# Kernel tuning notes

Measured on AMD Instinct MI355X. Metric: run time of the kernel, lower is better.

The kernel has to match this reference:

```python
import jax, jax.numpy as jnp
import numpy as np

N_CONCEPT = 15000  # graph has N_CONCEPT + 1 nodes
NNZ = 240016
EPS = 1e-12  # F.normalize eps


def setup_inputs() -> dict:
    key = jax.random.key(0)
    ks = jax.random.split(key, 10)
    B, S, E, O, D = 2048, 32, 1024, 1024, 1024
    s = 1.0 / np.sqrt(E)
    return {
        "data": jax.random.normal(ks[0], (B, S, E), jnp.float32),
        "seq_len": jax.random.randint(ks[1], (B,), 1, S + 1, jnp.int32),
        "conv_w": jax.random.normal(ks[2], (O, E), jnp.float32) * s,
        "conv_b": jax.random.normal(ks[3], (O,), jnp.float32) * s,
        "lin_w": jax.random.normal(ks[4], (D, O), jnp.float32) * s,
        "lin_b": jax.random.normal(ks[5], (D,), jnp.float32) * s,
        "gcn_bias": jnp.zeros((D,), jnp.float32),
        "H0": jax.random.normal(ks[6], (N_CONCEPT + 1, D), jnp.float32) * s,
        "indices": jax.random.randint(ks[7], (2, NNZ), 0, N_CONCEPT + 1, jnp.int32),
        "values": jax.random.uniform(ks[8], (NNZ,), jnp.float32),
    }


def reference(data, seq_len, conv_w, conv_b, lin_w, lin_b, gcn_bias, H0, indices, values):
    # --- CNN phrase encoder ---
    # conv1d kernel_size=1 == per-token linear: (B,S,E)x(O,E) -> (B,S,O)
    x = jax.nn.relu(jnp.einsum("bse,oe->bso", data, conv_w) + conv_b)
    x = jnp.max(x, axis=1)                              # max over sequence -> (B,O)
    x = jax.nn.relu(x @ lin_w.T + lin_b)                # (B,D)
    norm = jnp.linalg.norm(x, axis=1, keepdims=True)
    phrase = x / jnp.maximum(norm, EPS)                 # L2 normalize

    # --- sparse Laplacian GCN: L @ H0 + bias ---
    rows, cols = indices[0], indices[1]
    msgs = values[:, None] * H0[cols]                   # (nnz, D)
    graph = jax.ops.segment_sum(msgs, rows, num_segments=N_CONCEPT + 1) + gcn_bias

    # --- bilinear score: (B,D) @ (D, N+1) ---
    logits = phrase @ graph.T
    return logits
```

## Files before the change

kernel.cpp:

```cpp
#include <hip/hip_runtime.h>
#include <stdint.h>

typedef __attribute__((ext_vector_type(8))) __bf16 bf16x8;
typedef __attribute__((ext_vector_type(4))) float floatx4;

#define GLOBAL_AS __attribute__((address_space(1)))
#define LDS_AS __attribute__((address_space(3)))

#define CAP 96
#define N1 15001
#define NPAD 15104

__device__ __forceinline__ unsigned short f2bf(float x) {
  unsigned int u = __builtin_bit_cast(unsigned int, x);
  u += 0x7FFFu + ((u >> 16) & 1u);
  return (unsigned short)(u >> 16);
}
__device__ __forceinline__ unsigned int pk2(float lo, float hi) {
  return (unsigned)f2bf(lo) | ((unsigned)f2bf(hi) << 16);
}

__device__ __forceinline__ void stage_tile(const unsigned short* g, int ld, int row0, int k0,
                                           bf16x8* lds, int tid) {
  const int lane = tid & 63;
  const int w = tid >> 6;
#pragma unroll
  for (int j = 0; j < 2; ++j) {
    const int c = j * 256 + w * 64;
    const int kg = c >> 7;
    const int mbase = c & 127;
    const unsigned short* src = g + ((size_t)(row0 + mbase + lane) * ld + k0 + kg * 8);
    __builtin_amdgcn_global_load_lds((const GLOBAL_AS void*)src, (LDS_AS void*)(lds + c),
                                     16, 0, 0);
  }
}

template <int MODE>
__launch_bounds__(256, 2)
__global__ void gemm_bt(const void* __restrict__ Aptr,
                        const unsigned short* __restrict__ Bm,
                        const float* __restrict__ bias,
                        float* __restrict__ outF,
                        unsigned short* __restrict__ outU,
                        int nValid) {
  __shared__ bf16x8 As[512];
  __shared__ bf16x8 Bs[512];
  const int tid = threadIdx.x;
  const int lane = tid & 63;
  const int w = tid >> 6;
  const int wm = w >> 1, wn = w & 1;
  const int quad = lane >> 4, col = lane & 15;
  const int m0 = blockIdx.y * 128, n0 = blockIdx.x * 128;
  const int K = 1024;

  floatx4 acc[4][4];
#pragma unroll
  for (int a = 0; a < 4; ++a)
#pragma unroll
    for (int b = 0; b < 4; ++b) acc[a][b] = 0;

  for (int k0 = 0; k0 < K; k0 += 32) {
    __syncthreads();
    if (MODE == 0) {
      const int row = tid >> 1, kh = tid & 1;
      const float* src = (const float*)Aptr + (size_t)(m0 + row) * K + k0 + kh * 16;
      float4 v0 = ((const float4*)src)[0];
      float4 v1 = ((const float4*)src)[1];
      float4 v2 = ((const float4*)src)[2];
      float4 v3 = ((const float4*)src)[3];
      stage_tile(Bm, K, n0, k0, Bs, tid);
      uint4 c0, c1;
      c0.x = pk2(v0.x, v0.y); c0.y = pk2(v0.z, v0.w);
      c0.z = pk2(v1.x, v1.y); c0.w = pk2(v1.z, v1.w);
      c1.x = pk2(v2.x, v2.y); c1.y = pk2(v2.z, v2.w);
      c1.z = pk2(v3.x, v3.y); c1.w = pk2(v3.z, v3.w);
      ((uint4*)As)[(kh * 2) * 128 + row] = c0;
      ((uint4*)As)[(kh * 2 + 1) * 128 + row] = c1;
    } else {
      stage_tile((const unsigned short*)Aptr, K, m0, k0, As, tid);
      stage_tile(Bm, K, n0, k0, Bs, tid);
    }
    __syncthreads();
    bf16x8 af[4], bfr[4];
#pragma unroll
    for (int t = 0; t < 4; ++t) af[t] = As[quad * 128 + wm * 64 + t * 16 + col];
#pragma unroll
    for (int t = 0; t < 4; ++t) bfr[t] = Bs[quad * 128 + wn * 64 + t * 16 + col];
#pragma unroll
    for (int mt = 0; mt < 4; ++mt)
#pragma unroll
      for (int nt = 0; nt < 4; ++nt)
        acc[mt][nt] = __builtin_amdgcn_mfma_f32_16x16x32_bf16(af[mt], bfr[nt], acc[mt][nt], 0, 0, 0);
  }

  if (MODE == 0 || MODE == 3) {
    float bv[4];
#pragma unroll
    for (int nt = 0; nt < 4; ++nt) bv[nt] = bias[n0 + wn * 64 + nt * 16 + col];
#pragma unroll
    for (int g = 0; g < 2; ++g) {
#pragma unroll
      for (int nt = 0; nt < 4; ++nt) {
        float v = -3.4e38f;
#pragma unroll
        for (int mh = 0; mh < 2; ++mh) {
          const int mt = 2 * g + mh;
#pragma unroll
          for (int r = 0; r < 4; ++r) v = fmaxf(v, acc[mt][nt][r]);
        }
        v += bv[nt];
        v = fmaxf(v, __shfl_xor(v, 16, 64));
        v = fmaxf(v, __shfl_xor(v, 32, 64));
        v = fmaxf(v, 0.0f);
        if (quad == 0) {
          const int b = (m0 >> 5) + wm * 2 + g;
          outU[b * 1024 + n0 + wn * 64 + nt * 16 + col] = f2bf(v);
        }
      }
    }
  } else if (MODE == 1) {
    float bv[4];
#pragma unroll
    for (int nt = 0; nt < 4; ++nt) bv[nt] = bias[n0 + wn * 64 + nt * 16 + col];
#pragma unroll
    for (int mt = 0; mt < 4; ++mt)
#pragma unroll
      for (int r = 0; r < 4; ++r) {
        const int row = m0 + wm * 64 + mt * 16 + quad * 4 + r;
#pragma unroll
        for (int nt = 0; nt < 4; ++nt)
          outF[(size_t)row * 1024 + n0 + wn * 64 + nt * 16 + col] =
              fmaxf(acc[mt][nt][r] + bv[nt], 0.0f);
      }
  } else {
#pragma unroll
    for (int mt = 0; mt < 4; ++mt)
#pragma unroll
      for (int r = 0; r < 4; ++r) {
        const size_t row = m0 + wm * 64 + mt * 16 + quad * 4 + r;
#pragma unroll
        for (int nt = 0; nt < 4; ++nt) {
          const int cg = n0 + wn * 64 + nt * 16 + col;
          if (cg < nValid) outF[row * (size_t)nValid + cg] = acc[mt][nt][r];
        }
      }
  }
}

__global__ void f32_to_bf16(const float* __restrict__ in, unsigned short* __restrict__ out, int n4) {
  const int i = blockIdx.x * 256 + threadIdx.x;
  if (i >= n4) return;
  const float4 v = ((const float4*)in)[i];
  uint2 p;
  p.x = pk2(v.x, v.y);
  p.y = pk2(v.z, v.w);
  ((uint2*)out)[i] = p;
}

__global__ void bucket_fill(const int* __restrict__ rows, int nnz,
                            int* __restrict__ cnt, int* __restrict__ bucket) {
  const int e = blockIdx.x * 256 + threadIdx.x;
  if (e >= nnz) return;
  const int r = rows[e];
  if ((unsigned)r >= (unsigned)N1) return;
  const int pos = atomicAdd(&cnt[r], 1);
  if (pos < CAP) bucket[r * CAP + pos] = e;
}

__global__ void build_graph(const int* __restrict__ cols,
                            const float* __restrict__ values,
                            const float* __restrict__ H0,
                            const float* __restrict__ gbias,
                            const int* __restrict__ cnt,
                            const int* __restrict__ bucket,
                            unsigned short* __restrict__ graph) {
  __shared__ int s_col[CAP];
  __shared__ float s_val[CAP];
  const int r = blockIdx.x;
  const int t = threadIdx.x;
  int n = (r < N1) ? cnt[r] : 0;
  if (n > CAP) n = CAP;
  if (t < n) {
    const int e = bucket[r * CAP + t];
    s_col[t] = cols[e];
    s_val[t] = values[e];
  }
  __syncthreads();
  float4 a = *(const float4*)(gbias + t * 4);
  for (int i = 0; i < n; ++i) {
    const int c = s_col[i];
    const float f = s_val[i];
    const float4 hv = *(const float4*)(H0 + (size_t)c * 1024 + t * 4);
    a.x += f * hv.x;
    a.y += f * hv.y;
    a.z += f * hv.z;
    a.w += f * hv.w;
  }
  uint2 p;
  p.x = pk2(a.x, a.y);
  p.y = pk2(a.z, a.w);
  *(uint2*)(graph + (size_t)r * 1024 + t * 4) = p;
}

__global__ void normalize_rows(const float* __restrict__ x, unsigned short* __restrict__ phrase) {
  const int b = blockIdx.x;
  const int t = threadIdx.x;
  const float4 v = *(const float4*)(x + (size_t)b * 1024 + t * 4);
  float ss = v.x * v.x + v.y * v.y + v.z * v.z + v.w * v.w;
#pragma unroll
  for (int o = 32; o > 0; o >>= 1) ss += __shfl_down(ss, o, 64);
  __shared__ float sred[4];
  if ((t & 63) == 0) sred[t >> 6] = ss;
  __syncthreads();
  const float tot = sred[0] + sred[1] + sred[2] + sred[3];
  const float inv = 1.0f / fmaxf(sqrtf(tot), 1e-12f);
  uint2 p;
  p.x = pk2(v.x * inv, v.y * inv);
  p.y = pk2(v.z * inv, v.w * inv);
  *(uint2*)(phrase + (size_t)b * 1024 + t * 4) = p;
}

extern "C" void kernel_launch(void* const* d_in, const int* in_sizes, int n_in,
                              void* d_out, int out_size, void* d_ws, size_t ws_size,
                              hipStream_t stream) {
  const float* data   = (const float*)d_in[0];
  const float* conv_w = (const float*)d_in[2];
  const float* conv_b = (const float*)d_in[3];
  const float* lin_w  = (const float*)d_in[4];
  const float* lin_b  = (const float*)d_in[5];
  const float* gbias  = (const float*)d_in[6];
  const float* H0     = (const float*)d_in[7];
  const int* indices  = (const int*)d_in[8];
  const float* values = (const float*)d_in[9];
  float* out = (float*)d_out;

  const int NNZ = in_sizes[9];

  char* ws = (char*)d_ws;
  char* ws0 = ws;
  unsigned short* conv_wb = (unsigned short*)ws; ws += (size_t)1024 * 1024 * 2;
  unsigned short* lin_wb  = (unsigned short*)ws; ws += (size_t)1024 * 1024 * 2;
  unsigned short* pooled  = (unsigned short*)ws; ws += (size_t)2048 * 1024 * 2;
  float* xbuf             = (float*)ws;          ws += (size_t)2048 * 1024 * 4;
  unsigned short* phrase  = (unsigned short*)ws; ws += (size_t)2048 * 1024 * 2;
  unsigned short* graph   = (unsigned short*)ws; ws += (size_t)NPAD * 1024 * 2;
  int* cnt                = (int*)ws;            ws += (size_t)NPAD * 4;
  int* bucket             = (int*)ws;            ws += (size_t)NPAD * CAP * 4;

  const size_t dataBfBytes = (size_t)2048 * 32 * 1024 * 2;
  unsigned short* data_bf = nullptr;
  if (ws_size >= (size_t)(ws - ws0) + dataBfBytes) {
    data_bf = (unsigned short*)ws;
    ws += dataBfBytes;
  }

  f32_to_bf16<<<1024, 256, 0, stream>>>(conv_w, conv_wb, 1024 * 1024 / 4);
  f32_to_bf16<<<1024, 256, 0, stream>>>(lin_w, lin_wb, 1024 * 1024 / 4);

  hipMemsetAsync(cnt, 0, (size_t)NPAD * 4, stream);
  bucket_fill<<<(NNZ + 255) / 256, 256, 0, stream>>>(indices, NNZ, cnt, bucket);
  build_graph<<<NPAD, 256, 0, stream>>>(indices + NNZ, values, H0, gbias, cnt, bucket, graph);

  if (data_bf) {
    f32_to_bf16<<<(2048 * 32 * 1024 / 4 + 255) / 256, 256, 0, stream>>>(
        data, data_bf, 2048 * 32 * 1024 / 4);
    gemm_bt<3><<<dim3(8, 512), 256, 0, stream>>>(data_bf, conv_wb, conv_b, nullptr, pooled, 1024);
  } else {
    gemm_bt<0><<<dim3(8, 512), 256, 0, stream>>>(data, conv_wb, conv_b, nullptr, pooled, 1024);
  }
  gemm_bt<1><<<dim3(8, 16), 256, 0, stream>>>(pooled, lin_wb, lin_b, xbuf, nullptr, 1024);
  normalize_rows<<<2048, 256, 0, stream>>>(xbuf, phrase);

  gemm_bt<2><<<dim3(118, 16), 256, 0, stream>>>(phrase, graph, nullptr, out, nullptr, N1);
}
```

Baseline: 1.069 ms.

## Double-buffer GEMM LDS tiles and swizzle block order for L2 reuse

The shared A and B tiles become two buffers. The next K-slice is staged into the spare buffer while MFMAs run on the current one, which cuts the barriers per iteration from two to one and overlaps global loads with compute. Block indices are also remapped into groups of 8 rows when the grid height allows, so neighbouring blocks share operand tiles in L2. The cost is double the LDS per block, which could lower occupancy. In the fp32-A mode the loads still go through registers, so less of the load time is hidden there.

```diff
diff --git a/kernel.cpp b/kernel.cpp
--- a/kernel.cpp
+++ b/kernel.cpp
@@ -43,14 +43,22 @@
                         float* __restrict__ outF,
                         unsigned short* __restrict__ outU,
                         int nValid) {
-  __shared__ bf16x8 As[512];
-  __shared__ bf16x8 Bs[512];
+  __shared__ bf16x8 As[2][512];
+  __shared__ bf16x8 Bs[2][512];
   const int tid = threadIdx.x;
   const int lane = tid & 63;
   const int w = tid >> 6;
   const int wm = w >> 1, wn = w & 1;
   const int quad = lane >> 4, col = lane & 15;
-  const int m0 = blockIdx.y * 128, n0 = blockIdx.x * 128;
+
+  int bx = blockIdx.x, by = blockIdx.y;
+  if ((gridDim.y & 7) == 0) {
+    const unsigned L = (unsigned)by * gridDim.x + bx;
+    const unsigned i = L >> 3, xk = L & 7;
+    bx = i % gridDim.x;
+    by = (i / gridDim.x) * 8 + xk;
+  }
+  const int m0 = by * 128, n0 = bx * 128;
   const int K = 1024;
 
   floatx4 acc[4][4];
@@ -59,8 +67,7 @@
 #pragma unroll
     for (int b = 0; b < 4; ++b) acc[a][b] = 0;
 
-  for (int k0 = 0; k0 < K; k0 += 32) {
-    __syncthreads();
+  auto stage = [&](int buf, int k0) {
     if (MODE == 0) {
       const int row = tid >> 1, kh = tid & 1;
       const float* src = (const float*)Aptr + (size_t)(m0 + row) * K + k0 + kh * 16;
@@ -68,29 +75,36 @@
       float4 v1 = ((const float4*)src)[1];
       float4 v2 = ((const float4*)src)[2];
       float4 v3 = ((const float4*)src)[3];
-      stage_tile(Bm, K, n0, k0, Bs, tid);
+      stage_tile(Bm, K, n0, k0, Bs[buf], tid);
       uint4 c0, c1;
       c0.x = pk2(v0.x, v0.y); c0.y = pk2(v0.z, v0.w);
       c0.z = pk2(v1.x, v1.y); c0.w = pk2(v1.z, v1.w);
       c1.x = pk2(v2.x, v2.y); c1.y = pk2(v2.z, v2.w);
       c1.z = pk2(v3.x, v3.y); c1.w = pk2(v3.z, v3.w);
-      ((uint4*)As)[(kh * 2) * 128 + row] = c0;
-      ((uint4*)As)[(kh * 2 + 1) * 128 + row] = c1;
+      ((uint4*)As[buf])[(kh * 2) * 128 + row] = c0;
+      ((uint4*)As[buf])[(kh * 2 + 1) * 128 + row] = c1;
     } else {
-      stage_tile((const unsigned short*)Aptr, K, m0, k0, As, tid);
-      stage_tile(Bm, K, n0, k0, Bs, tid);
+      stage_tile((const unsigned short*)Aptr, K, m0, k0, As[buf], tid);
+      stage_tile(Bm, K, n0, k0, Bs[buf], tid);
     }
+  };
+
+  stage(0, 0);
+  int cur = 0;
+  for (int k0 = 0; k0 < K; k0 += 32) {
     __syncthreads();
+    if (k0 + 32 < K) stage(cur ^ 1, k0 + 32);
     bf16x8 af[4], bfr[4];
 #pragma unroll
-    for (int t = 0; t < 4; ++t) af[t] = As[quad * 128 + wm * 64 + t * 16 + col];
-#pragma unroll
-    for (int t = 0; t < 4; ++t) bfr[t] = Bs[quad * 128 + wn * 64 + t * 16 + col];
+    for (int t = 0; t < 4; ++t) af[t] = As[cur][quad * 128 + wm * 64 + t * 16 + col];
+#pragma unroll
+    for (int t = 0; t < 4; ++t) bfr[t] = Bs[cur][quad * 128 + wn * 64 + t * 16 + col];
 #pragma unroll
     for (int mt = 0; mt < 4; ++mt)
 #pragma unroll
       for (int nt = 0; nt < 4; ++nt)
         acc[mt][nt] = __builtin_amdgcn_mfma_f32_16x16x32_bf16(af[mt], bfr[nt], acc[mt][nt], 0, 0, 0);
+    cur ^= 1;
   }
 
   if (MODE == 0 || MODE == 3) {
```

Measured after the change: 1.022 ms. 1.05x faster.
